# Performance work log

Hardware: AMD Instinct MI355X
Metric: run time of the kernel (lower is better)

## Reference

```python
import jax, jax.numpy as jnp
import numpy as np
from jax import lax

N_NODES = 5000; N_EDGES = 160000; N_FEAT = 128; HIDDEN = 256
N_TPL = 10; N_TPL_NODES = 10; N_CLASSES = 8
ALPHA = 0.5          # FGW structure/feature trade-off
CG_ITERS = 5         # conditional-gradient (Frank-Wolfe) outer iterations
SINK_ITERS = 30      # log-domain Sinkhorn iterations (EMD surrogate)
SINK_REG = 0.02      # entropic reg relative to cost scale


def setup_inputs() -> dict:
    key = jax.random.key(0)
    ks = jax.random.split(key, 8)
    x = jax.random.normal(ks[0], (N_NODES, N_FEAT), jnp.float32)
    edge_index = jax.random.randint(ks[1], (2, N_EDGES), 0, N_NODES)
    W1 = jax.random.normal(ks[2], (N_FEAT, HIDDEN), jnp.float32) / np.sqrt(N_FEAT)
    b1 = jnp.zeros((HIDDEN,), jnp.float32)
    W2 = jax.random.normal(ks[3], (HIDDEN, N_FEAT), jnp.float32) / np.sqrt(HIDDEN)
    b2 = jnp.zeros((N_FEAT,), jnp.float32)
    templates = jax.random.uniform(ks[4], (N_TPL, N_TPL_NODES, N_TPL_NODES), jnp.float32)
    templates_features = jax.random.uniform(ks[5], (N_TPL, N_TPL_NODES, N_FEAT), jnp.float32)
    Wlin = jax.random.normal(ks[6], (N_TPL, N_CLASSES), jnp.float32) / np.sqrt(N_TPL)
    blin = jnp.zeros((N_CLASSES,), jnp.float32)
    return dict(x=x, edge_index=edge_index, W1=W1, b1=b1, W2=W2, b2=b2,
                templates=templates, templates_features=templates_features,
                Wlin=Wlin, blin=blin)


def gcn_conv(x, src, dst, W, b):
    # PyG GCNConv: x @ W, then D^-1/2 (A + I) D^-1/2 aggregation, then + b
    n = x.shape[0]
    loop = jnp.arange(n)
    s = jnp.concatenate([src, loop]); d = jnp.concatenate([dst, loop])
    deg = jax.ops.segment_sum(jnp.ones(s.shape[0], x.dtype), d, num_segments=n)
    dinv = lax.rsqrt(jnp.maximum(deg, 1.0))
    h = x @ W
    msg = h[s] * (dinv[s] * dinv[d])[:, None]
    return jax.ops.segment_sum(msg, d, num_segments=n) + b


def sinkhorn_log(G, logp, logq):
    # entropic OT in log domain as a jit-friendly surrogate for exact EMD
    scale = lax.stop_gradient(jnp.max(jnp.abs(G)) + 1e-9)
    mlogK = -G / (SINK_REG * scale)          # [n, m]
    f0 = jnp.zeros(G.shape[0], G.dtype); g0 = jnp.zeros(G.shape[1], G.dtype)
    def body(carry, _):
        f, g = carry
        g = logq - jax.nn.logsumexp(mlogK + f[:, None], axis=0)
        f = logp - jax.nn.logsumexp(mlogK + g[None, :], axis=1)
        return (f, g), None
    (f, g), _ = lax.scan(body, (f0, g0), None, length=SINK_ITERS)
    return jnp.exp(f[:, None] + mlogK + g[None, :])


def fgw2(C1, x, C2, F2):
    # Fused Gromov-Wasserstein distance (square loss), uniform weights,
    # conditional-gradient with fixed step 2/(t+2) and Sinkhorn LP surrogate.
    n, m = C1.shape[0], C2.shape[0]
    p = jnp.full((n,), 1.0 / n, x.dtype); q = jnp.full((m,), 1.0 / m, x.dtype)
    logp = jnp.log(p); logq = jnp.log(q)
    # squared-euclidean feature cost  [n, m]
    M = jnp.sum(x * x, 1)[:, None] + jnp.sum(F2 * F2, 1)[None, :] - 2.0 * x @ F2.T
    # square-loss GW decomposition: f1=a^2, f2=b^2, h1=a, h2=2b
    constC = ((C1 * C1) @ p)[:, None] + ((C2 * C2) @ q)[None, :]
    def tens(T):
        return constC - C1 @ T @ (2.0 * C2).T
    T = p[:, None] * q[None, :]
    for t in range(CG_ITERS):
        grad = (1.0 - ALPHA) * M + 2.0 * ALPHA * tens(T)
        Tnew = sinkhorn_log(grad, logp, logq)
        T = T + (2.0 / (t + 2.0)) * (Tnew - T)
    return (1.0 - ALPHA) * jnp.sum(M * T) + ALPHA * jnp.sum(tens(T) * T)


def reference(x, edge_index, W1, b1, W2, b2, templates, templates_features, Wlin, blin):
    src, dst = edge_index[0], edge_index[1]
    h = jax.nn.relu(gcn_conv(x, src, dst, W1, b1))
    h = gcn_conv(h, src, dst, W2, b2)           # [N, F]
    n = x.shape[0]
    C = jnp.zeros((n, n), x.dtype).at[src, dst].set(1.0)   # dense adjacency
    dists = jax.vmap(lambda Ct, Ft: fgw2(C, h, Ct, Ft))(templates, templates_features)  # [K]
    return dists @ Wlin + blin                  # [num_classes]
```

## Files before the change

### kernel.cpp

```cpp
#include <hip/hip_runtime.h>
#include <cstdint>

#define NND 5000
#define NE 160000
#define NF 128
#define NH 256
#define NT 10
#define MT 10
#define NC 8
#define NMAT (NND*MT)
#define ROWP 12
#define NMATP (NND*ROWP)
#define CG_ITERS 5
#define SINK_IT 30

#if __has_builtin(__builtin_amdgcn_update_dpp)
#define DPP_ADD(x, ctrl, rmask) \
    ((x) + __int_as_float(__builtin_amdgcn_update_dpp(0, __float_as_int(x), (ctrl), (rmask), 0xf, true)))
#define DPP_MAX(x, ctrl, rmask) \
    fmaxf((x), __int_as_float(__builtin_amdgcn_update_dpp(0, __float_as_int(x), (ctrl), (rmask), 0xf, true)))
__device__ __forceinline__ float wave_sum63(float x) {
    x = DPP_ADD(x, 0x111, 0xf);
    x = DPP_ADD(x, 0x112, 0xf);
    x = DPP_ADD(x, 0x114, 0xf);
    x = DPP_ADD(x, 0x118, 0xf);
    x = DPP_ADD(x, 0x142, 0xa);
    x = DPP_ADD(x, 0x143, 0xc);
    return x;
}
__device__ __forceinline__ float wave_max63(float x) {
    x = DPP_MAX(x, 0x111, 0xf);
    x = DPP_MAX(x, 0x112, 0xf);
    x = DPP_MAX(x, 0x114, 0xf);
    x = DPP_MAX(x, 0x118, 0xf);
    x = DPP_MAX(x, 0x142, 0xa);
    x = DPP_MAX(x, 0x143, 0xc);
    return x;
}
#else
__device__ __forceinline__ float wave_sum63(float x) {
#pragma unroll
    for (int off = 32; off; off >>= 1) x += __shfl_xor(x, off);
    return x;
}
__device__ __forceinline__ float wave_max63(float x) {
#pragma unroll
    for (int off = 32; off; off >>= 1) x = fmaxf(x, __shfl_xor(x, off));
    return x;
}
#endif

__device__ __forceinline__ float frcp(float x) {
#if __has_builtin(__builtin_amdgcn_rcpf)
    return __builtin_amdgcn_rcpf(x);
#else
    return 1.f / x;
#endif
}


__global__ void k_edge1(const int* __restrict__ src, const int* __restrict__ dst,
                        int* __restrict__ cntD, unsigned* __restrict__ bitmap,
                        int* __restrict__ cntS, unsigned char* __restrict__ keep) {
    for (int e = blockIdx.x*blockDim.x + threadIdx.x; e < NE; e += gridDim.x*blockDim.x) {
        int s = src[e], d = dst[e];
        atomicAdd(&cntD[d], 1);
        int key = s * NND + d;
        unsigned bit = 1u << (key & 31);
        unsigned old = atomicOr(&bitmap[key >> 5], bit);
        if (!(old & bit)) { keep[e] = 1; atomicAdd(&cntS[s], 1); }
        else keep[e] = 0;
    }
}

__global__ void k_exscan2(const int* __restrict__ cntD, int* __restrict__ rpD,
                          float* __restrict__ dinv,
                          const int* __restrict__ cntS, int* __restrict__ rpS,
                          float* __restrict__ c1row,
                          const float* __restrict__ tpl, float* __restrict__ c2row,
                          float* __restrict__ rsT) {
    const int T = 1024;
    int tid = threadIdx.x;
    if (blockIdx.x == 2) {
        if (tid < NT * MT) {
            int t = tid / MT, j = tid % MT;
            float s = 0.f, rs = 0.f;
            for (int k = 0; k < MT; k++) {
                float v = tpl[t * 100 + j * 10 + k];
                s += v * v; rs += v;
            }
            c2row[tid] = s * (1.f / MT);
            rsT[tid] = rs;
        }
        return;
    }
    const int* cnt = blockIdx.x ? cntS : cntD;
    int* rp = blockIdx.x ? rpS : rpD;
    int C = (NND + T - 1) / T;
    int begin = tid * C, end = begin + C; if (end > NND) end = NND; if (begin > NND) begin = NND;
    int s = 0;
    for (int i = begin; i < end; i++) s += cnt[i];
    __shared__ int part[1024];
    part[tid] = s; __syncthreads();
    for (int off = 1; off < T; off <<= 1) {
        int v = (tid >= off) ? part[tid - off] : 0;
        __syncthreads();
        part[tid] += v;
        __syncthreads();
    }
    int run = part[tid] - s;
    for (int i = begin; i < end; i++) { rp[i] = run; run += cnt[i]; }
    if (tid == T - 1) rp[NND] = part[T - 1];
    if (blockIdx.x == 0)
        for (int i = begin; i < end; i++) dinv[i] = rsqrtf((float)(cnt[i] + 1));
    else
        for (int i = begin; i < end; i++) c1row[i] = (float)cnt[i] * (1.f / NND);
}

__global__ void k_scatter2(const int* __restrict__ src, const int* __restrict__ dst,
                           const unsigned char* __restrict__ keep,
                           const int* __restrict__ rpD, int* __restrict__ cur1,
                           int* __restrict__ csrS, float* __restrict__ csrC,
                           const float* __restrict__ dinv,
                           const int* __restrict__ rpS, int* __restrict__ cur2,
                           int* __restrict__ csrD) {
    for (int e = blockIdx.x*blockDim.x + threadIdx.x; e < NE; e += gridDim.x*blockDim.x) {
        int s = src[e], d = dst[e];
        int pos = rpD[d] + atomicAdd(&cur1[d], 1);
        csrS[pos] = s;
        csrC[pos] = dinv[s] * dinv[d];
        if (keep[e]) {
            int p2 = rpS[s] + atomicAdd(&cur2[s], 1);
            csrD[p2] = d;
        }
    }
}


__global__ __launch_bounds__(256) void k_gemm(const float* __restrict__ A,
                                              const float* __restrict__ B,
                                              float* __restrict__ C, int M, int N, int K,
                                              const float* __restrict__ bias, int relu) {
    const int BM = 64, BN = 64, BK = 16;
    __shared__ float As[BK][BM + 4];
    __shared__ float Bs[BK][BN];
    int tid = threadIdx.x;
    int row0 = blockIdx.y * BM, col0 = blockIdx.x * BN;
    int tx = tid % 16, ty = tid / 16;
    float acc[4][4] = {};
    for (int k0 = 0; k0 < K; k0 += BK) {
#pragma unroll
        for (int l = 0; l < 4; l++) {
            int idx = tid + l * 256;
            int r = idx / BK, kk = idx % BK;
            int gr = row0 + r;
            As[kk][r] = (gr < M) ? A[(size_t)gr * K + k0 + kk] : 0.f;
        }
#pragma unroll
        for (int l = 0; l < 4; l++) {
            int idx = tid + l * 256;
            int kk = idx / BN, c = idx % BN;
            Bs[kk][c] = B[(size_t)(k0 + kk) * N + col0 + c];
        }
        __syncthreads();
#pragma unroll
        for (int kk = 0; kk < BK; kk++) {
            float a[4], b[4];
#pragma unroll
            for (int i = 0; i < 4; i++) a[i] = As[kk][ty * 4 + i];
#pragma unroll
            for (int j = 0; j < 4; j++) b[j] = Bs[kk][tx * 4 + j];
#pragma unroll
            for (int i = 0; i < 4; i++)
#pragma unroll
                for (int j = 0; j < 4; j++) acc[i][j] += a[i] * b[j];
        }
        __syncthreads();
    }
#pragma unroll
    for (int i = 0; i < 4; i++) {
        int gr = row0 + ty * 4 + i;
        if (gr < M) {
#pragma unroll
            for (int j = 0; j < 4; j++) {
                int gc = col0 + tx * 4 + j;
                float o = acc[i][j];
                if (bias) o += bias[gc];
                if (relu) o = fmaxf(o, 0.f);
                C[(size_t)gr * N + gc] = o;
            }
        }
    }
}

__global__ __launch_bounds__(256) void k_aggregate(const float4* __restrict__ hin4,
                            float4* __restrict__ hout4, const int* __restrict__ rp,
                            const int* __restrict__ csrS, const float* __restrict__ csrC,
                            const float* __restrict__ dinv) {
    int v = blockIdx.x * 8 + (threadIdx.x >> 5);
    int l = threadIdx.x & 31;
    float dv = dinv[v];
    float sc = dv * dv;
    float4 a = hin4[(size_t)v * 32 + l];
    float4 acc = make_float4(a.x * sc, a.y * sc, a.z * sc, a.w * sc);
    int e0 = rp[v], e1 = rp[v + 1];
    for (int e = e0; e < e1; e++) {
        int s = csrS[e];
        float c = csrC[e];
        float4 hv = hin4[(size_t)s * 32 + l];
        acc.x = fmaf(hv.x, c, acc.x);
        acc.y = fmaf(hv.y, c, acc.y);
        acc.z = fmaf(hv.z, c, acc.z);
        acc.w = fmaf(hv.w, c, acc.w);
    }
    hout4[(size_t)v * 32 + l] = acc;
}

__global__ __launch_bounds__(128) void k_fuse(const float* __restrict__ t2,
                    const float* __restrict__ b2,
                    const int* __restrict__ rp, const int* __restrict__ csrS,
                    const float* __restrict__ csrC, const float* __restrict__ dinv,
                    const float* __restrict__ tplF,
                    const float* __restrict__ c1row, const int* __restrict__ cntS,
                    const float* __restrict__ c2row, const float* __restrict__ rsT,
                    float* __restrict__ Mm, float* __restrict__ G,
                    float* __restrict__ T, float* __restrict__ pmax) {
    int i = blockIdx.x;
    int tid = threadIdx.x;
    int lane = tid & 63, w = tid >> 6;
    __shared__ float hrow[NF];
    __shared__ float part[2];
    __shared__ float sMax[112];
    float dv = dinv[i];
    float acc = t2[(size_t)i * NF + tid] * (dv * dv);
    int e0 = rp[i], e1 = rp[i + 1];
    for (int e = e0; e < e1; e++)
        acc = fmaf(t2[(size_t)csrS[e] * NF + tid], csrC[e], acc);
    acc += b2[tid];
    hrow[tid] = acc;
    float ps = wave_sum63(acc * acc);
    if (lane == 63) part[w] = ps;
    __syncthreads();
    float sx = part[0] + part[1];
    int c = tid;
    if (c < NT * MT) {
        const float4* Fc = (const float4*)(tplF + (size_t)c * NF);
        const float4* hr = (const float4*)hrow;
        float dot = 0.f, nrm = 0.f;
#pragma unroll 8
        for (int f = 0; f < NF / 4; f++) {
            float4 fv = Fc[f];
            float4 hq = hr[f];
            dot = fmaf(hq.x, fv.x, dot); dot = fmaf(hq.y, fv.y, dot);
            dot = fmaf(hq.z, fv.z, dot); dot = fmaf(hq.w, fv.w, dot);
            nrm = fmaf(fv.x, fv.x, nrm); nrm = fmaf(fv.y, fv.y, nrm);
            nrm = fmaf(fv.z, fv.z, nrm); nrm = fmaf(fv.w, fv.w, nrm);
        }
        float m = sx + nrm - 2.f * dot;
        int t = c / MT, j = c % MT;
        size_t base = (size_t)t * NMATP + (size_t)i * ROWP + j;
        Mm[base] = m;
        T[base] = 1.f / (float)NMAT;
        float g = 0.5f * m + c1row[i] + c2row[c]
                - ((float)cntS[i] * (1.f / NMAT)) * (2.f * rsT[c]);
        G[base] = g;
        sMax[c] = fabsf(g);
    }
    __syncthreads();
    if (tid < NT) {
        float m = sMax[tid * 10];
#pragma unroll
        for (int k = 1; k < 10; k++) m = fmaxf(m, sMax[tid * 10 + k]);
        pmax[(size_t)tid * NND + i] = m;
    }
}


__global__ __launch_bounds__(256) void k_grad(const float* __restrict__ T, const float* __restrict__ Mm,
                                              const float* __restrict__ c1row, const float* __restrict__ c2row,
                                              const float* __restrict__ tpl,
                                              const int* __restrict__ rpS, const int* __restrict__ csrD,
                                              float* __restrict__ G, unsigned* __restrict__ scaleBits) {
    int t = blockIdx.y;
    int tid = threadIdx.x;
    __shared__ float tC2[100];
    if (tid < 100) tC2[tid] = 2.f * tpl[t * 100 + tid];
    __syncthreads();
    int i = blockIdx.x * 256 + tid;
    float amax = 0.f;
    if (i < NND) {
        const float* Tt = T + (size_t)t * NMATP;
        float4 A0 = make_float4(0.f,0.f,0.f,0.f);
        float4 A1 = make_float4(0.f,0.f,0.f,0.f);
        float2 A2 = make_float2(0.f,0.f);
        int e0 = rpS[i], e1 = rpS[i + 1];
        for (int e = e0; e < e1; e++) {
            int k = csrD[e];
            const float4* Tk = (const float4*)(Tt + (size_t)k * ROWP);
            float4 x0 = Tk[0], x1 = Tk[1];
            float2 x2 = ((const float2*)Tk)[4];
            A0.x += x0.x; A0.y += x0.y; A0.z += x0.z; A0.w += x0.w;
            A1.x += x1.x; A1.y += x1.y; A1.z += x1.z; A1.w += x1.w;
            A2.x += x2.x; A2.y += x2.y;
        }
        float L[10] = {A0.x, A0.y, A0.z, A0.w, A1.x, A1.y, A1.z, A1.w, A2.x, A2.y};
        const float4* Mt4 = (const float4*)(Mm + (size_t)t * NMATP + (size_t)i * ROWP);
        float4 m0 = Mt4[0], m1 = Mt4[1];
        float2 m2 = ((const float2*)Mt4)[4];
        float m[10] = {m0.x, m0.y, m0.z, m0.w, m1.x, m1.y, m1.z, m1.w, m2.x, m2.y};
        float c1 = c1row[i];
        float g[10];
#pragma unroll
        for (int j = 0; j < MT; j++) {
            float s = 0.f;
#pragma unroll
            for (int k = 0; k < MT; k++) s = fmaf(L[k], tC2[j * 10 + k], s);
            g[j] = 0.5f * m[j] + (c1 + c2row[t * 10 + j] - s);
            amax = fmaxf(amax, fabsf(g[j]));
        }
        float4* Gt4 = (float4*)(G + (size_t)t * NMATP + (size_t)i * ROWP);
        Gt4[0] = make_float4(g[0], g[1], g[2], g[3]);
        Gt4[1] = make_float4(g[4], g[5], g[6], g[7]);
        ((float2*)Gt4)[4] = make_float2(g[8], g[9]);
    }
    __shared__ float red[256];
    red[tid] = amax; __syncthreads();
    for (int off = 128; off > 0; off >>= 1) {
        if (tid < off) red[tid] = fmaxf(red[tid], red[tid + off]);
        __syncthreads();
    }
    if (tid == 0) atomicMax(&scaleBits[t], __float_as_uint(red[0]));
}

__global__ __attribute__((amdgpu_flat_work_group_size(512, 512), amdgpu_waves_per_eu(2, 2)))
void k_sinkhorn(const float* __restrict__ G,
                const unsigned* __restrict__ scaleBits,
                const float* __restrict__ pmax,
                float* __restrict__ T, float step) {
    int t = blockIdx.x;
    int tid = threadIdx.x;
    int lane = tid & 63, w = tid >> 6;

    __shared__ float wred[8][10];
    __shared__ float4 vbc4[3];
    __shared__ float scsh;

    float sc;
    if (pmax) {
        const float* pm = pmax + (size_t)t * NND;
        float m = 0.f;
        for (int k = tid; k < NND; k += 512) m = fmaxf(m, pm[k]);
        m = wave_max63(m);
        if (lane == 63) wred[w][0] = m;
        __syncthreads();
        if (tid == 0) {
            float mm = wred[0][0];
#pragma unroll
            for (int q = 1; q < 8; q++) mm = fmaxf(mm, wred[q][0]);
            scsh = mm;
        }
        __syncthreads();
        sc = scsh;
    } else {
        sc = __uint_as_float(scaleBits[t]);
    }
    float inv = -1.f / (0.02f * (sc + 1e-9f));
    const float* Gt = G + (size_t)t * NMATP;
    float* Tt = T + (size_t)t * NMATP;

    float Kf[10][10];
    float u[10];
#pragma unroll
    for (int r = 0; r < 10; r++) {
        int i = tid + r * 512;
        if (i < NND) {
            u[r] = 1.f;
            const float4* Gr = (const float4*)(Gt + (size_t)i * ROWP);
            float4 ga = Gr[0], gb = Gr[1];
            float2 gc = ((const float2*)Gr)[4];
            Kf[r][0] = __expf(ga.x * inv); Kf[r][1] = __expf(ga.y * inv);
            Kf[r][2] = __expf(ga.z * inv); Kf[r][3] = __expf(ga.w * inv);
            Kf[r][4] = __expf(gb.x * inv); Kf[r][5] = __expf(gb.y * inv);
            Kf[r][6] = __expf(gb.z * inv); Kf[r][7] = __expf(gb.w * inv);
            Kf[r][8] = __expf(gc.x * inv); Kf[r][9] = __expf(gc.y * inv);
        } else {
            u[r] = 0.f;
#pragma unroll
            for (int j = 0; j < 10; j++) Kf[r][j] = 0.f;
        }
    }

    float vv[10];

    for (int it = 0; it < SINK_IT; it++) {
        float S[10];
#pragma unroll
        for (int j = 0; j < 10; j++) S[j] = 0.f;
#pragma unroll
        for (int r = 0; r < 10; r++) {
            float ur = u[r];
#pragma unroll
            for (int j = 0; j < 10; j++) S[j] = fmaf(Kf[r][j], ur, S[j]);
        }
#pragma unroll
        for (int j = 0; j < 10; j++) {
            float s = wave_sum63(S[j]);
            if (lane == 63) wred[w][j] = s;
        }
        __syncthreads();
        if (tid < 10) {
            float s = 0.f;
#pragma unroll
            for (int q = 0; q < 8; q++) s += wred[q][tid];
            ((float*)vbc4)[tid] = 0.1f * frcp(fmaxf(s, 1e-30f));
        }
        __syncthreads();
        {
            float4 a = vbc4[0], b = vbc4[1], c = vbc4[2];
            vv[0]=a.x; vv[1]=a.y; vv[2]=a.z; vv[3]=a.w;
            vv[4]=b.x; vv[5]=b.y; vv[6]=b.z; vv[7]=b.w;
            vv[8]=c.x; vv[9]=c.y;
        }
#pragma unroll
        for (int r = 0; r < 10; r++) {
            float R = 0.f;
#pragma unroll
            for (int j = 0; j < 10; j++) R = fmaf(Kf[r][j], vv[j], R);
            u[r] = 2e-4f * frcp(fmaxf(R, 1e-30f));
        }
    }

#pragma unroll
    for (int r = 0; r < 10; r++) {
        int i = tid + r * 512;
        if (i < NND) {
            float ur = u[r];
            float4* Tr4 = (float4*)(Tt + (size_t)i * ROWP);
            float4 t0 = Tr4[0], t1 = Tr4[1];
            float2 t2v = ((float2*)Tr4)[4];
            t0.x += step * (ur * Kf[r][0] * vv[0] - t0.x);
            t0.y += step * (ur * Kf[r][1] * vv[1] - t0.y);
            t0.z += step * (ur * Kf[r][2] * vv[2] - t0.z);
            t0.w += step * (ur * Kf[r][3] * vv[3] - t0.w);
            t1.x += step * (ur * Kf[r][4] * vv[4] - t1.x);
            t1.y += step * (ur * Kf[r][5] * vv[5] - t1.y);
            t1.z += step * (ur * Kf[r][6] * vv[6] - t1.z);
            t1.w += step * (ur * Kf[r][7] * vv[7] - t1.w);
            t2v.x += step * (ur * Kf[r][8] * vv[8] - t2v.x);
            t2v.y += step * (ur * Kf[r][9] * vv[9] - t2v.y);
            Tr4[0] = t0; Tr4[1] = t1;
            ((float2*)Tr4)[4] = t2v;
        }
    }
}


__global__ __launch_bounds__(256) void k_final(const float* __restrict__ T, const float* __restrict__ Mm,
                                               const float* __restrict__ c1row, const float* __restrict__ c2row,
                                               const float* __restrict__ tpl,
                                               const int* __restrict__ rpS, const int* __restrict__ csrD,
                                               double* __restrict__ dd, int* __restrict__ done,
                                               const float* __restrict__ Wlin,
                                               const float* __restrict__ blin,
                                               float* __restrict__ out) {
    int t = blockIdx.y;
    int tid = threadIdx.x;
    __shared__ float tC2[100];
    if (tid < 100) tC2[tid] = 2.f * tpl[t * 100 + tid];
    __syncthreads();
    int i = blockIdx.x * 256 + tid;
    double msum = 0.0, tsum = 0.0;
    if (i < NND) {
        const float* Tt = T + (size_t)t * NMATP;
        float4 A0 = make_float4(0.f,0.f,0.f,0.f);
        float4 A1 = make_float4(0.f,0.f,0.f,0.f);
        float2 A2 = make_float2(0.f,0.f);
        int e0 = rpS[i], e1 = rpS[i + 1];
        for (int e = e0; e < e1; e++) {
            int k = csrD[e];
            const float4* Tk = (const float4*)(Tt + (size_t)k * ROWP);
            float4 x0 = Tk[0], x1 = Tk[1];
            float2 x2 = ((const float2*)Tk)[4];
            A0.x += x0.x; A0.y += x0.y; A0.z += x0.z; A0.w += x0.w;
            A1.x += x1.x; A1.y += x1.y; A1.z += x1.z; A1.w += x1.w;
            A2.x += x2.x; A2.y += x2.y;
        }
        float L[10] = {A0.x, A0.y, A0.z, A0.w, A1.x, A1.y, A1.z, A1.w, A2.x, A2.y};
        const float4* Mt4 = (const float4*)(Mm + (size_t)t * NMATP + (size_t)i * ROWP);
        float4 m0 = Mt4[0], m1 = Mt4[1];
        float2 m2 = ((const float2*)Mt4)[4];
        float m[10] = {m0.x, m0.y, m0.z, m0.w, m1.x, m1.y, m1.z, m1.w, m2.x, m2.y};
        const float4* Ti4 = (const float4*)(Tt + (size_t)i * ROWP);
        float4 tv0 = Ti4[0], tv1 = Ti4[1];
        float2 tv2 = ((const float2*)Ti4)[4];
        float Tv[10] = {tv0.x, tv0.y, tv0.z, tv0.w, tv1.x, tv1.y, tv1.z, tv1.w, tv2.x, tv2.y};
        float c1 = c1row[i];
#pragma unroll
        for (int j = 0; j < MT; j++) {
            float s = 0.f;
#pragma unroll
            for (int k = 0; k < MT; k++) s = fmaf(L[k], tC2[j * 10 + k], s);
            float ts = c1 + c2row[t * 10 + j] - s;
            msum += (double)(m[j] * Tv[j]);
            tsum += (double)(ts * Tv[j]);
        }
    }
    __shared__ double r1[256], r2[256];
    r1[tid] = msum; r2[tid] = tsum; __syncthreads();
    for (int off = 128; off > 0; off >>= 1) {
        if (tid < off) { r1[tid] += r1[tid + off]; r2[tid] += r2[tid + off]; }
        __syncthreads();
    }
    if (tid == 0) {
        atomicAdd(&dd[t * 2], r1[0]);
        atomicAdd(&dd[t * 2 + 1], r2[0]);
        __threadfence();
        int prev = atomicAdd(done, 1);
        if (prev == 20 * NT - 1) {
            __threadfence();
            float ds[NT];
#pragma unroll
            for (int k = 0; k < NT; k++) {
                unsigned long long b0 = __hip_atomic_load((unsigned long long*)&dd[2*k],
                                        __ATOMIC_RELAXED, __HIP_MEMORY_SCOPE_AGENT);
                unsigned long long b1 = __hip_atomic_load((unsigned long long*)&dd[2*k+1],
                                        __ATOMIC_RELAXED, __HIP_MEMORY_SCOPE_AGENT);
                ds[k] = 0.5f * (float)(__longlong_as_double(b0) + __longlong_as_double(b1));
            }
#pragma unroll
            for (int c = 0; c < NC; c++) {
                float o = blin[c];
#pragma unroll
                for (int k = 0; k < NT; k++) o = fmaf(ds[k], Wlin[k * NC + c], o);
                out[c] = o;
            }
        }
    }
}


extern "C" void kernel_launch(void* const* d_in, const int* in_sizes, int n_in,
                              void* d_out, int out_size, void* d_ws, size_t ws_size,
                              hipStream_t stream) {
    const float* x    = (const float*)d_in[0];
    const int*   ei   = (const int*)d_in[1];
    const int*   src  = ei;
    const int*   dst  = ei + NE;
    const float* W1   = (const float*)d_in[2];
    const float* b1   = (const float*)d_in[3];
    const float* W2   = (const float*)d_in[4];
    const float* b2   = (const float*)d_in[5];
    const float* tpl  = (const float*)d_in[6];
    const float* tplF = (const float*)d_in[7];
    const float* Wlin = (const float*)d_in[8];
    const float* blin = (const float*)d_in[9];
    float* out = (float*)d_out;

    char* w = (char*)d_ws;
    size_t off = 0;
    auto alloc = [&](size_t b) -> char* {
        off = (off + 255) & ~(size_t)255;
        char* p = w + off; off += b; return p;
    };
    float* bufA = (float*)alloc((size_t)NND * NH * 4);
    float* bufB = (float*)alloc((size_t)NND * NH * 4);
    float* Mm   = (float*)alloc((size_t)NT * NMATP * 4);
    float* T    = (float*)alloc((size_t)NT * NMATP * 4);
    float* G    = (float*)alloc((size_t)NT * NMATP * 4);
    float* pmax = (float*)alloc((size_t)NT * NND * 4);
    int* cntD = (int*)alloc((size_t)NND * 4);
    int* cntS = (int*)alloc((size_t)NND * 4);
    int* cur1 = (int*)alloc((size_t)NND * 4);
    int* cur2 = (int*)alloc((size_t)NND * 4);
    double* dd = (double*)alloc((size_t)NT * 2 * 8);
    int* done = (int*)alloc(4);
    unsigned* scaleArr = (unsigned*)alloc((size_t)CG_ITERS * NT * 4);
    unsigned* bitmap = (unsigned*)alloc((size_t)781250 * 4);
    char* zend = w + off;
    int* rpD  = (int*)alloc((size_t)(NND + 1) * 4);
    int* rpS  = (int*)alloc((size_t)(NND + 1) * 4);
    int* csrS = (int*)alloc((size_t)NE * 4);
    float* csrC = (float*)alloc((size_t)NE * 4);
    int* csrD2 = (int*)alloc((size_t)NE * 4);
    unsigned char* keep = (unsigned char*)alloc((size_t)NE);
    float* dinv  = (float*)alloc((size_t)NND * 4);
    float* c1row = (float*)alloc((size_t)NND * 4);
    float* c2row = (float*)alloc((size_t)100 * 4);
    float* rsT   = (float*)alloc((size_t)100 * 4);

    hipMemsetAsync(cntD, 0, (size_t)(zend - (char*)cntD), stream);

    k_edge1<<<625, 256, 0, stream>>>(src, dst, cntD, bitmap, cntS, keep);
    k_exscan2<<<3, 1024, 0, stream>>>(cntD, rpD, dinv, cntS, rpS, c1row, tpl, c2row, rsT);
    k_scatter2<<<625, 256, 0, stream>>>(src, dst, keep, rpD, cur1, csrS, csrC, dinv,
                                        rpS, cur2, csrD2);

    k_aggregate<<<625, 256, 0, stream>>>((const float4*)x, (float4*)bufA,
                                         rpD, csrS, csrC, dinv);
    k_gemm<<<dim3(NH / 64, (NND + 63) / 64), 256, 0, stream>>>(bufA, W1, bufB, NND, NH, NF, b1, 1);
    k_gemm<<<dim3(NF / 64, (NND + 63) / 64), 256, 0, stream>>>(bufB, W2, bufA, NND, NF, NH, nullptr, 0);

    k_fuse<<<NND, 128, 0, stream>>>(bufA, b2, rpD, csrS, csrC, dinv, tplF,
                                    c1row, cntS, c2row, rsT, Mm, G, T, pmax);

    for (int t = 0; t < CG_ITERS; t++) {
        unsigned* sb = scaleArr + t * NT;
        if (t > 0)
            k_grad<<<dim3(20, NT), 256, 0, stream>>>(T, Mm, c1row, c2row, tpl, rpS, csrD2, G, sb);
        float step = 2.f / (float)(t + 2);
        k_sinkhorn<<<NT, 512, 0, stream>>>(G, sb, (t == 0) ? pmax : nullptr, T, step);
    }

    k_final<<<dim3(20, NT), 256, 0, stream>>>(T, Mm, c1row, c2row, tpl, rpS, csrD2,
                                              dd, done, Wlin, blin, out);
}
```

Baseline: 658.8 us.

## Unroll edge gathers by two, compact G layout, widen GEMM K tile

Raises the GEMM K-tile from 16 to 32 so each tile loads more data. Unrolls the CSR neighbor loops in aggregate, fuse, grad and final kernels by two so more independent gather loads are in flight at once. Stores the gradient matrix G unpadded, with 10 floats per row instead of 12, cutting its footprint and read traffic in the Sinkhorn kernel at the cost of narrower float2 accesses. The larger K tile roughly doubles GEMM shared-memory use, which may lower occupancy.

```diff
diff --git a/kernel.cpp b/kernel.cpp
--- a/kernel.cpp
+++ b/kernel.cpp
@@ -141,7 +141,7 @@
                                               const float* __restrict__ B,
                                               float* __restrict__ C, int M, int N, int K,
                                               const float* __restrict__ bias, int relu) {
-    const int BM = 64, BN = 64, BK = 16;
+    const int BM = 64, BN = 64, BK = 32;
     __shared__ float As[BK][BM + 4];
     __shared__ float Bs[BK][BN];
     int tid = threadIdx.x;
@@ -150,14 +150,14 @@
     float acc[4][4] = {};
     for (int k0 = 0; k0 < K; k0 += BK) {
 #pragma unroll
-        for (int l = 0; l < 4; l++) {
+        for (int l = 0; l < 8; l++) {
             int idx = tid + l * 256;
             int r = idx / BK, kk = idx % BK;
             int gr = row0 + r;
             As[kk][r] = (gr < M) ? A[(size_t)gr * K + k0 + kk] : 0.f;
         }
 #pragma unroll
-        for (int l = 0; l < 4; l++) {
+        for (int l = 0; l < 8; l++) {
             int idx = tid + l * 256;
             int kk = idx / BN, c = idx % BN;
             Bs[kk][c] = B[(size_t)(k0 + kk) * N + col0 + c];
@@ -204,14 +204,22 @@
     float4 a = hin4[(size_t)v * 32 + l];
     float4 acc = make_float4(a.x * sc, a.y * sc, a.z * sc, a.w * sc);
     int e0 = rp[v], e1 = rp[v + 1];
-    for (int e = e0; e < e1; e++) {
-        int s = csrS[e];
-        float c = csrC[e];
-        float4 hv = hin4[(size_t)s * 32 + l];
-        acc.x = fmaf(hv.x, c, acc.x);
-        acc.y = fmaf(hv.y, c, acc.y);
-        acc.z = fmaf(hv.z, c, acc.z);
-        acc.w = fmaf(hv.w, c, acc.w);
+    int e = e0;
+    for (; e + 1 < e1; e += 2) {
+        int s0 = csrS[e],   s1 = csrS[e+1];
+        float c0 = csrC[e], c1 = csrC[e+1];
+        float4 h0 = hin4[(size_t)s0 * 32 + l];
+        float4 h1 = hin4[(size_t)s1 * 32 + l];
+        acc.x = fmaf(h0.x, c0, acc.x); acc.y = fmaf(h0.y, c0, acc.y);
+        acc.z = fmaf(h0.z, c0, acc.z); acc.w = fmaf(h0.w, c0, acc.w);
+        acc.x = fmaf(h1.x, c1, acc.x); acc.y = fmaf(h1.y, c1, acc.y);
+        acc.z = fmaf(h1.z, c1, acc.z); acc.w = fmaf(h1.w, c1, acc.w);
+    }
+    if (e < e1) {
+        int s0 = csrS[e]; float c0 = csrC[e];
+        float4 h0 = hin4[(size_t)s0 * 32 + l];
+        acc.x = fmaf(h0.x, c0, acc.x); acc.y = fmaf(h0.y, c0, acc.y);
+        acc.z = fmaf(h0.z, c0, acc.z); acc.w = fmaf(h0.w, c0, acc.w);
     }
     hout4[(size_t)v * 32 + l] = acc;
 }
@@ -234,8 +242,16 @@
     float dv = dinv[i];
     float acc = t2[(size_t)i * NF + tid] * (dv * dv);
     int e0 = rp[i], e1 = rp[i + 1];
-    for (int e = e0; e < e1; e++)
-        acc = fmaf(t2[(size_t)csrS[e] * NF + tid], csrC[e], acc);
+    int e = e0;
+    for (; e + 1 < e1; e += 2) {
+        int s0 = csrS[e], s1 = csrS[e+1];
+        float c0 = csrC[e], c1 = csrC[e+1];
+        float h0 = t2[(size_t)s0 * NF + tid];
+        float h1 = t2[(size_t)s1 * NF + tid];
+        acc = fmaf(h0, c0, acc);
+        acc = fmaf(h1, c1, acc);
+    }
+    if (e < e1) acc = fmaf(t2[(size_t)csrS[e] * NF + tid], csrC[e], acc);
     acc += b2[tid];
     hrow[tid] = acc;
     float ps = wave_sum63(acc * acc);
@@ -258,12 +274,12 @@
         }
         float m = sx + nrm - 2.f * dot;
         int t = c / MT, j = c % MT;
-        size_t base = (size_t)t * NMATP + (size_t)i * ROWP + j;
-        Mm[base] = m;
-        T[base] = 1.f / (float)NMAT;
+        size_t baseP = (size_t)t * NMATP + (size_t)i * ROWP + j;
+        Mm[baseP] = m;
+        T[baseP] = 1.f / (float)NMAT;
         float g = 0.5f * m + c1row[i] + c2row[c]
                 - ((float)cntS[i] * (1.f / NMAT)) * (2.f * rsT[c]);
-        G[base] = g;
+        G[(size_t)t * NMAT + (size_t)i * MT + j] = g;
         sMax[c] = fabsf(g);
     }
     __syncthreads();
@@ -294,14 +310,27 @@
         float4 A1 = make_float4(0.f,0.f,0.f,0.f);
         float2 A2 = make_float2(0.f,0.f);
         int e0 = rpS[i], e1 = rpS[i + 1];
-        for (int e = e0; e < e1; e++) {
-            int k = csrD[e];
-            const float4* Tk = (const float4*)(Tt + (size_t)k * ROWP);
-            float4 x0 = Tk[0], x1 = Tk[1];
-            float2 x2 = ((const float2*)Tk)[4];
-            A0.x += x0.x; A0.y += x0.y; A0.z += x0.z; A0.w += x0.w;
-            A1.x += x1.x; A1.y += x1.y; A1.z += x1.z; A1.w += x1.w;
-            A2.x += x2.x; A2.y += x2.y;
+        int e = e0;
+        for (; e + 1 < e1; e += 2) {
+            int ka = csrD[e], kb = csrD[e+1];
+            const float4* Ta = (const float4*)(Tt + (size_t)ka * ROWP);
+            const float4* Tb = (const float4*)(Tt + (size_t)kb * ROWP);
+            float4 a0 = Ta[0], a1 = Ta[1];
+            float2 a2 = ((const float2*)Ta)[4];
+            float4 b0 = Tb[0], b1 = Tb[1];
+            float2 b2v = ((const float2*)Tb)[4];
+            A0.x += a0.x + b0.x; A0.y += a0.y + b0.y; A0.z += a0.z + b0.z; A0.w += a0.w + b0.w;
+            A1.x += a1.x + b1.x; A1.y += a1.y + b1.y; A1.z += a1.z + b1.z; A1.w += a1.w + b1.w;
+            A2.x += a2.x + b2v.x; A2.y += a2.y + b2v.y;
+        }
+        if (e < e1) {
+            int ka = csrD[e];
+            const float4* Ta = (const float4*)(Tt + (size_t)ka * ROWP);
+            float4 a0 = Ta[0], a1 = Ta[1];
+            float2 a2 = ((const float2*)Ta)[4];
+            A0.x += a0.x; A0.y += a0.y; A0.z += a0.z; A0.w += a0.w;
+            A1.x += a1.x; A1.y += a1.y; A1.z += a1.z; A1.w += a1.w;
+            A2.x += a2.x; A2.y += a2.y;
         }
         float L[10] = {A0.x, A0.y, A0.z, A0.w, A1.x, A1.y, A1.z, A1.w, A2.x, A2.y};
         const float4* Mt4 = (const float4*)(Mm + (size_t)t * NMATP + (size_t)i * ROWP);
@@ -318,10 +347,9 @@
             g[j] = 0.5f * m[j] + (c1 + c2row[t * 10 + j] - s);
             amax = fmaxf(amax, fabsf(g[j]));
         }
-        float4* Gt4 = (float4*)(G + (size_t)t * NMATP + (size_t)i * ROWP);
-        Gt4[0] = make_float4(g[0], g[1], g[2], g[3]);
-        Gt4[1] = make_float4(g[4], g[5], g[6], g[7]);
-        ((float2*)Gt4)[4] = make_float2(g[8], g[9]);
+        float2* Gt2 = (float2*)(G + (size_t)t * NMAT + (size_t)i * MT);
+#pragma unroll
+        for (int h = 0; h < 5; h++) Gt2[h] = make_float2(g[2*h], g[2*h+1]);
     }
     __shared__ float red[256];
     red[tid] = amax; __syncthreads();
@@ -365,7 +393,7 @@
         sc = __uint_as_float(scaleBits[t]);
     }
     float inv = -1.f / (0.02f * (sc + 1e-9f));
-    const float* Gt = G + (size_t)t * NMATP;
+    const float* Gt = G + (size_t)t * NMAT;
     float* Tt = T + (size_t)t * NMATP;
 
     float Kf[10][10];
@@ -375,14 +403,13 @@
         int i = tid + r * 512;
         if (i < NND) {
             u[r] = 1.f;
-            const float4* Gr = (const float4*)(Gt + (size_t)i * ROWP);
-            float4 ga = Gr[0], gb = Gr[1];
-            float2 gc = ((const float2*)Gr)[4];
-            Kf[r][0] = __expf(ga.x * inv); Kf[r][1] = __expf(ga.y * inv);
-            Kf[r][2] = __expf(ga.z * inv); Kf[r][3] = __expf(ga.w * inv);
-            Kf[r][4] = __expf(gb.x * inv); Kf[r][5] = __expf(gb.y * inv);
-            Kf[r][6] = __expf(gb.z * inv); Kf[r][7] = __expf(gb.w * inv);
-            Kf[r][8] = __expf(gc.x * inv); Kf[r][9] = __expf(gc.y * inv);
+            const float2* Gr = (const float2*)(Gt + (size_t)i * 10);
+#pragma unroll
+            for (int h = 0; h < 5; h++) {
+                float2 g = Gr[h];
+                Kf[r][2*h]   = __expf(g.x * inv);
+                Kf[r][2*h+1] = __expf(g.y * inv);
+            }
         } else {
             u[r] = 0.f;
 #pragma unroll
@@ -476,14 +503,27 @@
         float4 A1 = make_float4(0.f,0.f,0.f,0.f);
         float2 A2 = make_float2(0.f,0.f);
         int e0 = rpS[i], e1 = rpS[i + 1];
-        for (int e = e0; e < e1; e++) {
-            int k = csrD[e];
-            const float4* Tk = (const float4*)(Tt + (size_t)k * ROWP);
-            float4 x0 = Tk[0], x1 = Tk[1];
-            float2 x2 = ((const float2*)Tk)[4];
-            A0.x += x0.x; A0.y += x0.y; A0.z += x0.z; A0.w += x0.w;
-            A1.x += x1.x; A1.y += x1.y; A1.z += x1.z; A1.w += x1.w;
-            A2.x += x2.x; A2.y += x2.y;
+        int e = e0;
+        for (; e + 1 < e1; e += 2) {
+            int ka = csrD[e], kb = csrD[e+1];
+            const float4* Ta = (const float4*)(Tt + (size_t)ka * ROWP);
+            const float4* Tb = (const float4*)(Tt + (size_t)kb * ROWP);
+            float4 a0 = Ta[0], a1 = Ta[1];
+            float2 a2 = ((const float2*)Ta)[4];
+            float4 b0 = Tb[0], b1 = Tb[1];
+            float2 b2v = ((const float2*)Tb)[4];
+            A0.x += a0.x + b0.x; A0.y += a0.y + b0.y; A0.z += a0.z + b0.z; A0.w += a0.w + b0.w;
+            A1.x += a1.x + b1.x; A1.y += a1.y + b1.y; A1.z += a1.z + b1.z; A1.w += a1.w + b1.w;
+            A2.x += a2.x + b2v.x; A2.y += a2.y + b2v.y;
+        }
+        if (e < e1) {
+            int ka = csrD[e];
+            const float4* Ta = (const float4*)(Tt + (size_t)ka * ROWP);
+            float4 a0 = Ta[0], a1 = Ta[1];
+            float2 a2 = ((const float2*)Ta)[4];
+            A0.x += a0.x; A0.y += a0.y; A0.z += a0.z; A0.w += a0.w;
+            A1.x += a1.x; A1.y += a1.y; A1.z += a1.z; A1.w += a1.w;
+            A2.x += a2.x; A2.y += a2.y;
         }
         float L[10] = {A0.x, A0.y, A0.z, A0.w, A1.x, A1.y, A1.z, A1.w, A2.x, A2.y};
         const float4* Mt4 = (const float4*)(Mm + (size_t)t * NMATP + (size_t)i * ROWP);
@@ -566,7 +606,7 @@
     float* bufB = (float*)alloc((size_t)NND * NH * 4);
     float* Mm   = (float*)alloc((size_t)NT * NMATP * 4);
     float* T    = (float*)alloc((size_t)NT * NMATP * 4);
-    float* G    = (float*)alloc((size_t)NT * NMATP * 4);
+    float* G    = (float*)alloc((size_t)NT * NMAT * 4);
     float* pmax = (float*)alloc((size_t)NT * NND * 4);
     int* cntD = (int*)alloc((size_t)NND * 4);
     int* cntS = (int*)alloc((size_t)NND * 4);
```

After: 627.6 us. 4.7% less time.
